# Performance work log

Hardware: AMD Instinct MI355X
Metric: run time of the kernel (lower is better)

Reference implementation:

```python
import jax, jax.numpy as jnp
import numpy as np
import math

D_MODEL = 2048
NUM_HEADS = 16
D_FF = 8192
HEAD_DIM = D_MODEL // NUM_HEADS
EPS = 1e-5


def _xavier(key, out_f, in_f):
    std = math.sqrt(2.0 / (in_f + out_f))
    return jax.random.normal(key, (out_f, in_f), dtype=jnp.float32) * std


def setup_inputs() -> dict:
    key = jax.random.key(0)
    ks = jax.random.split(key, 8)
    x = jax.random.normal(ks[0], (2, 2048, D_MODEL), dtype=jnp.float32)
    return {
        "x": x,
        "Wq": _xavier(ks[1], D_MODEL, D_MODEL),
        "Wk": _xavier(ks[2], D_MODEL, D_MODEL),
        "Wv": _xavier(ks[3], D_MODEL, D_MODEL),
        "Wo": _xavier(ks[4], D_MODEL, D_MODEL),
        "W1": _xavier(ks[5], D_FF, D_MODEL),
        "W2": _xavier(ks[6], D_MODEL, D_FF),
        "g1": jnp.ones((D_MODEL,), jnp.float32),
        "b1": jnp.zeros((D_MODEL,), jnp.float32),
        "g2": jnp.ones((D_MODEL,), jnp.float32),
        "b2": jnp.zeros((D_MODEL,), jnp.float32),
    }


def _ternary(w):
    # per-tensor abs-mean threshold -> {-1, 0, 1}
    abs_w = jnp.abs(w)
    thr = jnp.mean(abs_w)
    return jnp.where(abs_w > thr, jnp.sign(w), jnp.zeros_like(w))


def _tlin(x, w):
    # F.linear with ternarized weight [out, in], no bias
    return jnp.einsum("bsi,oi->bso", x, _ternary(w))


def _layernorm(x, g, b):
    mu = jnp.mean(x, axis=-1, keepdims=True)
    var = jnp.mean(jnp.square(x - mu), axis=-1, keepdims=True)
    return (x - mu) * jax.lax.rsqrt(var + EPS) * g + b


def reference(x, Wq, Wk, Wv, Wo, W1, W2, g1, b1, g2, b2):
    B, S, D = x.shape
    H, Hd = NUM_HEADS, HEAD_DIM
    q = _tlin(x, Wq).reshape(B, S, H, Hd).transpose(0, 2, 1, 3)  # bhsd
    k = _tlin(x, Wk).reshape(B, S, H, Hd).transpose(0, 2, 1, 3)
    v = _tlin(x, Wv).reshape(B, S, H, Hd).transpose(0, 2, 1, 3)
    scores = jnp.einsum("bhqd,bhkd->bhqk", q, k) / math.sqrt(Hd)
    probs = jax.nn.softmax(scores, axis=-1)
    attn = jnp.einsum("bhqk,bhkd->bhqd", probs, v)
    attn = attn.transpose(0, 2, 1, 3).reshape(B, S, D)
    attn = _tlin(attn, Wo)
    x = _layernorm(x + attn, g1, b1)  # dropout is identity in eval
    ff = _tlin(jax.nn.relu(_tlin(x, W1)), W2)
    x = _layernorm(x + ff, g2, b2)
    return x
```

## Files before the change

kernel.cpp:

```cpp
#include <hip/hip_runtime.h>
#include <hip/hip_bf16.h>

typedef __bf16 bf16_t;
typedef __bf16 bf16x8 __attribute__((ext_vector_type(8)));
typedef __bf16 bf16x4 __attribute__((ext_vector_type(4)));
typedef float f32x4 __attribute__((ext_vector_type(4)));
typedef int i32x4 __attribute__((ext_vector_type(4)));

__device__ __forceinline__ f32x4 mfma16(bf16x8 a, bf16x8 b, f32x4 c) {
  return __builtin_amdgcn_mfma_f32_16x16x32_bf16(a, b, c, 0, 0, 0);
}

__device__ __forceinline__ void gload16(const void* g, void* l) {
  __builtin_amdgcn_global_load_lds(
      (const __attribute__((address_space(1))) void*)g,
      (__attribute__((address_space(3))) void*)l, 16, 0, 0);
}

__global__ void abssum_all(const float* __restrict__ W0, const float* __restrict__ W1_,
                           const float* __restrict__ W2_, const float* __restrict__ W3,
                           const float* __restrict__ W4, const float* __restrict__ W5,
                           double* __restrict__ partial) {
  __shared__ double sd[256];
  const int w = blockIdx.y, tid = threadIdx.x;
  const float* W = (w == 0) ? W0 : (w == 1) ? W1_ : (w == 2) ? W2_ : (w == 3) ? W3 : (w == 4) ? W4 : W5;
  const int n4 = (w < 4) ? 1048576 : 4194304;
  double s = 0.0;
  for (int i = blockIdx.x * 256 + tid; i < n4; i += 262144) {
    float4 v = ((const float4*)W)[i];
    s += (double)fabsf(v.x); s += (double)fabsf(v.y);
    s += (double)fabsf(v.z); s += (double)fabsf(v.w);
  }
  sd[tid] = s; __syncthreads();
  for (int st = 128; st > 0; st >>= 1) { if (tid < st) sd[tid] += sd[tid + st]; __syncthreads(); }
  if (tid == 0) partial[w * 1024 + blockIdx.x] = sd[0];
}

__global__ void abssum_fin(const double* __restrict__ partial, double* __restrict__ sums) {
  __shared__ double sd[256];
  const int tid = threadIdx.x;
  const double* p = partial + blockIdx.x * 1024;
  double s = p[tid] + p[tid + 256] + p[tid + 512] + p[tid + 768];
  sd[tid] = s; __syncthreads();
  for (int st = 128; st > 0; st >>= 1) { if (tid < st) sd[tid] += sd[tid + st]; __syncthreads(); }
  if (tid == 0) sums[blockIdx.x] = sd[0];
}

__global__ void ternarize4(const float* __restrict__ W0, const float* __restrict__ W1_,
                           const float* __restrict__ W2_, const float* __restrict__ W3,
                           bf16_t* __restrict__ out, const double* __restrict__ sums) {
  const int w = blockIdx.x >> 12;
  const float* W = (w == 0) ? W0 : (w == 1) ? W1_ : (w == 2) ? W2_ : W3;
  const double thr = sums[w] / 4194304.0;
  const int i = (blockIdx.x & 4095) * 256 + threadIdx.x;
  float4 v = ((const float4*)W)[i];
  bf16x4 o;
  float t;
  t = ((double)fabsf(v.x) > thr) ? (v.x > 0.f ? 1.f : -1.f) : 0.f; o[0] = (bf16_t)t;
  t = ((double)fabsf(v.y) > thr) ? (v.y > 0.f ? 1.f : -1.f) : 0.f; o[1] = (bf16_t)t;
  t = ((double)fabsf(v.z) > thr) ? (v.z > 0.f ? 1.f : -1.f) : 0.f; o[2] = (bf16_t)t;
  t = ((double)fabsf(v.w) > thr) ? (v.w > 0.f ? 1.f : -1.f) : 0.f; o[3] = (bf16_t)t;
  *(bf16x4*)&out[(size_t)w * 4194304 + (size_t)i * 4] = o;
}

__global__ void ternarize_k(const float* __restrict__ W, bf16_t* __restrict__ out,
                            const double* __restrict__ sum, double n) {
  const double thr = sum[0] / n;
  const int i = blockIdx.x * 256 + threadIdx.x;
  float4 v = ((const float4*)W)[i];
  bf16x4 o;
  float t;
  t = ((double)fabsf(v.x) > thr) ? (v.x > 0.f ? 1.f : -1.f) : 0.f; o[0] = (bf16_t)t;
  t = ((double)fabsf(v.y) > thr) ? (v.y > 0.f ? 1.f : -1.f) : 0.f; o[1] = (bf16_t)t;
  t = ((double)fabsf(v.z) > thr) ? (v.z > 0.f ? 1.f : -1.f) : 0.f; o[2] = (bf16_t)t;
  t = ((double)fabsf(v.w) > thr) ? (v.w > 0.f ? 1.f : -1.f) : 0.f; o[3] = (bf16_t)t;
  *(bf16x4*)&out[(size_t)i * 4] = o;
}

__global__ void split_x_k(const float* __restrict__ X, bf16_t* __restrict__ xh, bf16_t* __restrict__ xl) {
  const int i = blockIdx.x * 256 + threadIdx.x;
  float4 v = ((const float4*)X)[i];
  bf16x4 h, l;
  h[0] = (bf16_t)v.x; l[0] = (bf16_t)(v.x - (float)h[0]);
  h[1] = (bf16_t)v.y; l[1] = (bf16_t)(v.y - (float)h[1]);
  h[2] = (bf16_t)v.z; l[2] = (bf16_t)(v.z - (float)h[2]);
  h[3] = (bf16_t)v.w; l[3] = (bf16_t)(v.w - (float)h[3]);
  *(bf16x4*)&xh[(size_t)i * 4] = h;
  *(bf16x4*)&xl[(size_t)i * 4] = l;
}

template <int EPI, bool SPLITA>
__global__ __launch_bounds__(512, 2) void gemmP(
    const bf16_t* __restrict__ Ah, const bf16_t* __restrict__ Al,
    const bf16_t* __restrict__ Bw,
    void* __restrict__ C0, void* __restrict__ C1,
    int M, int N, int K) {
  constexpr int BM = SPLITA ? 64 : 128;
  constexpr int MREP = SPLITA ? 2 : 4;
  constexpr int ABUF = BM * 64;
  constexpr int BBUF = 256 * 64;
  __shared__ __align__(16) bf16_t sA[3][ABUF];
  __shared__ __align__(16) bf16_t sA2[SPLITA ? 3 : 1][SPLITA ? ABUF : 8];
  __shared__ __align__(16) bf16_t sB[3][BBUF];

  const int tid = threadIdx.x;
  const int wid = tid >> 6, lane = tid & 63, lr = lane & 15, lg = lane >> 4;
  const int wr = wid >> 2, wc = wid & 3;
  const size_t Ks = (size_t)K;

  const int nwg = gridDim.x * gridDim.y;
  const int bid0 = blockIdx.y * gridDim.x + blockIdx.x;
  const int swz = (bid0 & 7) * (nwg >> 3) + (bid0 >> 3);
  const int bx = swz % gridDim.x, by = swz / gridDim.x;
  const size_t m0 = (size_t)by * BM, n0 = (size_t)bx * 256;
  const int nt = K / 64;

  f32x4 acc[MREP][4] = {};

  auto STAGEH = [&](int bi, int kt, int half) {
    const size_t ko = (size_t)kt * 64;
    if (half == 0) {
#pragma unroll
      for (int i = 0; i < BM / 64; i++) {
        const int t = i * 512 + tid;
        const int r = t >> 3;
        const int su = (t & 7) ^ (r & 7);
        const int lo = (i * 512 + wid * 64) * 8;
        gload16(Ah + (m0 + r) * Ks + ko + su * 8, (void*)&sA[bi][lo]);
        if constexpr (SPLITA) gload16(Al + (m0 + r) * Ks + ko + su * 8, (void*)&sA2[bi][lo]);
      }
      {
        const int r = tid >> 3;
        const int su = (tid & 7) ^ (r & 7);
        gload16(Bw + (n0 + r) * Ks + ko + su * 8, (void*)&sB[bi][(wid * 64) * 8]);
      }
    } else {
#pragma unroll
      for (int i = 1; i < 4; i++) {
        const int t = i * 512 + tid;
        const int r = t >> 3;
        const int su = (t & 7) ^ (r & 7);
        gload16(Bw + (n0 + r) * Ks + ko + su * 8, (void*)&sB[bi][(i * 512 + wid * 64) * 8]);
      }
    }
  };
  auto LDA = [&](const bf16_t* base, int m, int k) -> bf16x8 {
    const int row = wr * (BM / 2) + m * 16 + lr;
    const int u = (k * 4 + lg) ^ (lr & 7);
    return *(const bf16x8*)&base[row * 64 + u * 8];
  };
  auto LDB = [&](const bf16_t* base, int n, int k) -> bf16x8 {
    const int row = wc * 64 + n * 16 + lr;
    const int u = (k * 4 + lg) ^ (lr & 7);
    return *(const bf16x8*)&base[row * 64 + u * 8];
  };

  STAGEH(0, 0, 0); STAGEH(0, 0, 1);
  STAGEH(1, 1, 0); STAGEH(1, 1, 1);
  asm volatile("s_waitcnt vmcnt(6)" ::: "memory");
  __builtin_amdgcn_s_barrier();

  int bc = 0, bs = 2;
  for (int kt = 0; kt < nt; kt++) {
    const bool pf = (kt + 2 < nt);
    bf16x8 a[MREP][2], bfr[4][2];
#pragma unroll
    for (int m = 0; m < MREP; m++)
#pragma unroll
      for (int k = 0; k < 2; k++) a[m][k] = LDA(&sA[bc][0], m, k);
    if constexpr (SPLITA) {
#pragma unroll
      for (int n = 0; n < 4; n++)
#pragma unroll
        for (int k = 0; k < 2; k++) bfr[n][k] = LDB(&sB[bc][0], n, k);
    } else {
#pragma unroll
      for (int n = 0; n < 2; n++)
#pragma unroll
        for (int k = 0; k < 2; k++) bfr[n][k] = LDB(&sB[bc][0], n, k);
    }
    if (pf) STAGEH(bs, kt + 2, 0);
    __builtin_amdgcn_s_barrier();
    asm volatile("s_waitcnt lgkmcnt(0)" ::: "memory");
    __builtin_amdgcn_sched_barrier(0);
    __builtin_amdgcn_s_setprio(1);
    if constexpr (SPLITA) {
#pragma unroll
      for (int k = 0; k < 2; k++)
#pragma unroll
        for (int m = 0; m < MREP; m++)
#pragma unroll
          for (int n = 0; n < 4; n++) acc[m][n] = mfma16(a[m][k], bfr[n][k], acc[m][n]);
    } else {
#pragma unroll
      for (int k = 0; k < 2; k++)
#pragma unroll
        for (int m = 0; m < MREP; m++)
#pragma unroll
          for (int n = 0; n < 2; n++) acc[m][n] = mfma16(a[m][k], bfr[n][k], acc[m][n]);
    }
    __builtin_amdgcn_s_setprio(0);
    __builtin_amdgcn_s_barrier();
    if constexpr (SPLITA) {
#pragma unroll
      for (int m = 0; m < MREP; m++)
#pragma unroll
        for (int k = 0; k < 2; k++) a[m][k] = LDA(&sA2[bc][0], m, k);
    } else {
#pragma unroll
      for (int n = 0; n < 2; n++)
#pragma unroll
        for (int k = 0; k < 2; k++) bfr[n + 2][k] = LDB(&sB[bc][0], n + 2, k);
    }
    if (pf) STAGEH(bs, kt + 2, 1);
    if (kt + 1 < nt) {
      if (pf) asm volatile("s_waitcnt vmcnt(6)" ::: "memory");
      else    asm volatile("s_waitcnt vmcnt(0)" ::: "memory");
    }
    __builtin_amdgcn_s_barrier();
    asm volatile("s_waitcnt lgkmcnt(0)" ::: "memory");
    __builtin_amdgcn_sched_barrier(0);
    __builtin_amdgcn_s_setprio(1);
    if constexpr (SPLITA) {
#pragma unroll
      for (int k = 0; k < 2; k++)
#pragma unroll
        for (int m = 0; m < MREP; m++)
#pragma unroll
          for (int n = 0; n < 4; n++) acc[m][n] = mfma16(a[m][k], bfr[n][k], acc[m][n]);
    } else {
#pragma unroll
      for (int k = 0; k < 2; k++)
#pragma unroll
        for (int m = 0; m < MREP; m++)
#pragma unroll
          for (int n = 0; n < 2; n++) acc[m][n + 2] = mfma16(a[m][k], bfr[n + 2][k], acc[m][n + 2]);
    }
    __builtin_amdgcn_s_setprio(0);
    __builtin_amdgcn_s_barrier();
    bc = (bc + 1 == 3) ? 0 : bc + 1;
    bs = (bs + 1 == 3) ? 0 : bs + 1;
  }

  const int row0 = (int)m0 + wr * (BM / 2), colb = (int)n0 + wc * 64;
#pragma unroll
  for (int m = 0; m < MREP; m++)
#pragma unroll
    for (int n = 0; n < 4; n++)
#pragma unroll
      for (int j = 0; j < 4; j++) {
        const int r = row0 + m * 16 + lg * 4 + j;
        const int c = colb + n * 16 + lr;
        const float v = acc[m][n][j];
        if constexpr (EPI == 0) {
          bf16_t hi = (bf16_t)v;
          ((bf16_t*)C0)[(size_t)r * N + c] = hi;
          ((bf16_t*)C1)[(size_t)r * N + c] = (bf16_t)(v - (float)hi);
        } else if constexpr (EPI == 1) {
          const int bb = r >> 11, ss = r & 2047;
          ((bf16_t*)C0)[((size_t)bb * 2048 + c) * 2048 + ss] = (bf16_t)v;
        } else if constexpr (EPI == 2) {
          ((float*)C0)[(size_t)r * N + c] = v;
        } else {
          ((bf16_t*)C0)[(size_t)r * N + c] = (bf16_t)fmaxf(v, 0.f);
        }
      }
  (void)M;
}

template <int EPI>
__global__ __launch_bounds__(512, 2) void gemm256(
    const bf16_t* __restrict__ A, const bf16_t* __restrict__ Bw,
    void* __restrict__ C0, int M, int N, int K) {
  __shared__ __align__(16) bf16_t sA[2][256 * 64];
  __shared__ __align__(16) bf16_t sB[2][256 * 64];
  const int tid = threadIdx.x;
  const int wid = tid >> 6, lane = tid & 63, lr = lane & 15, lg = lane >> 4;
  const int wr = wid >> 2, wc = wid & 3;
  const size_t Ks = (size_t)K;
  const int nwg = gridDim.x * gridDim.y;
  const int bid0 = blockIdx.y * gridDim.x + blockIdx.x;
  const int swz = (bid0 & 7) * (nwg >> 3) + (bid0 >> 3);
  const int bx = swz % gridDim.x, by = swz / gridDim.x;
  const size_t m0 = (size_t)by * 256, n0 = (size_t)bx * 256;
  const int nt = K / 64;
  const bf16_t* Abase = A + m0 * Ks;
  const bf16_t* Bbase = Bw + n0 * Ks;

  f32x4 acc[8][4] = {};

  auto SG = [&](const bf16_t* base, bf16_t* dst, int kt, int h) {
    const size_t ko = (size_t)kt * 64;
#pragma unroll
    for (int i = 0; i < 2; i++) {
      const int e = (2 * h + i) * 512 + tid;
      const int r = e >> 3;
      const int su = (tid & 7) ^ (r & 7);
      gload16(base + (size_t)r * Ks + ko + su * 8,
              (void*)&dst[((2 * h + i) * 512 + wid * 64) * 8]);
    }
  };
  auto LDA = [&](int bi, int m, int k) -> bf16x8 {
    const int row = wr * 128 + m * 16 + lr;
    const int u = (k * 4 + lg) ^ (lr & 7);
    return *(const bf16x8*)&sA[bi][row * 64 + u * 8];
  };
  auto LDB = [&](int bi, int n, int k) -> bf16x8 {
    const int row = wc * 64 + n * 16 + lr;
    const int u = (k * 4 + lg) ^ (lr & 7);
    return *(const bf16x8*)&sB[bi][row * 64 + u * 8];
  };

  SG(Abase, sA[0], 0, 0); SG(Abase, sA[0], 0, 1);
  SG(Bbase, sB[0], 0, 0); SG(Bbase, sB[0], 0, 1);
  SG(Bbase, sB[1], 1, 0); SG(Bbase, sB[1], 1, 1); SG(Abase, sA[1], 1, 0);
  asm volatile("s_waitcnt vmcnt(6)" ::: "memory");
  __builtin_amdgcn_s_barrier();

  for (int kt = 0; kt < nt; kt++) {
    const int bi = kt & 1, bn = bi ^ 1;
    bf16x8 a[4][2], b[4][2];
#pragma unroll
    for (int m = 0; m < 4; m++)
#pragma unroll
      for (int k = 0; k < 2; k++) a[m][k] = LDA(bi, m, k);
#pragma unroll
    for (int n = 0; n < 2; n++)
#pragma unroll
      for (int k = 0; k < 2; k++) b[n][k] = LDB(bi, n, k);
    if (kt + 1 < nt) SG(Abase, sA[bn], kt + 1, 1);
    __builtin_amdgcn_s_barrier();
    asm volatile("s_waitcnt lgkmcnt(0)" ::: "memory");
    __builtin_amdgcn_sched_barrier(0);
    __builtin_amdgcn_s_setprio(1);
#pragma unroll
    for (int k = 0; k < 2; k++)
#pragma unroll
      for (int m = 0; m < 4; m++)
#pragma unroll
        for (int n = 0; n < 2; n++) acc[m][n] = mfma16(a[m][k], b[n][k], acc[m][n]);
    __builtin_amdgcn_s_setprio(0);
    __builtin_amdgcn_s_barrier();
#pragma unroll
    for (int n = 0; n < 2; n++)
#pragma unroll
      for (int k = 0; k < 2; k++) b[n + 2][k] = LDB(bi, n + 2, k);
    if (kt + 2 < nt) SG(Bbase, sB[bi], kt + 2, 0);
    __builtin_amdgcn_s_barrier();
    asm volatile("s_waitcnt lgkmcnt(0)" ::: "memory");
    __builtin_amdgcn_sched_barrier(0);
    __builtin_amdgcn_s_setprio(1);
#pragma unroll
    for (int k = 0; k < 2; k++)
#pragma unroll
      for (int m = 0; m < 4; m++)
#pragma unroll
        for (int n = 0; n < 2; n++) acc[m][n + 2] = mfma16(a[m][k], b[n + 2][k], acc[m][n + 2]);
    __builtin_amdgcn_s_setprio(0);
    __builtin_amdgcn_s_barrier();
#pragma unroll
    for (int m = 0; m < 4; m++)
#pragma unroll
      for (int k = 0; k < 2; k++) a[m][k] = LDA(bi, m + 4, k);
    if (kt + 2 < nt) SG(Bbase, sB[bi], kt + 2, 1);
    __builtin_amdgcn_s_barrier();
    asm volatile("s_waitcnt lgkmcnt(0)" ::: "memory");
    __builtin_amdgcn_sched_barrier(0);
    __builtin_amdgcn_s_setprio(1);
#pragma unroll
    for (int k = 0; k < 2; k++)
#pragma unroll
      for (int m = 0; m < 4; m++)
#pragma unroll
        for (int n = 0; n < 2; n++) acc[m + 4][n + 2] = mfma16(a[m][k], b[n + 2][k], acc[m + 4][n + 2]);
    __builtin_amdgcn_s_setprio(0);
    __builtin_amdgcn_s_barrier();
    if (kt + 2 < nt) SG(Abase, sA[bi], kt + 2, 0);
    __builtin_amdgcn_s_setprio(1);
#pragma unroll
    for (int k = 0; k < 2; k++)
#pragma unroll
      for (int m = 0; m < 4; m++)
#pragma unroll
        for (int n = 0; n < 2; n++) acc[m + 4][n] = mfma16(a[m][k], b[n][k], acc[m + 4][n]);
    __builtin_amdgcn_s_setprio(0);
    if (kt + 1 < nt) {
      if (kt + 2 < nt) asm volatile("s_waitcnt vmcnt(6)" ::: "memory");
      else             asm volatile("s_waitcnt vmcnt(0)" ::: "memory");
    }
    __builtin_amdgcn_s_barrier();
  }

  const int row0 = (int)m0 + wr * 128, colb = (int)n0 + wc * 64;
#pragma unroll
  for (int m = 0; m < 8; m++)
#pragma unroll
    for (int n = 0; n < 4; n++)
#pragma unroll
      for (int j = 0; j < 4; j++) {
        const int r = row0 + m * 16 + lg * 4 + j;
        const int c = colb + n * 16 + lr;
        const float v = acc[m][n][j];
        if constexpr (EPI == 2) {
          ((float*)C0)[(size_t)r * N + c] = v;
        } else {
          ((bf16_t*)C0)[(size_t)r * N + c] = (bf16_t)fmaxf(v, 0.f);
        }
      }
  (void)M;
}

__global__ __launch_bounds__(256, 2) void attn_k(
    const bf16_t* __restrict__ qh, const bf16_t* __restrict__ ql,
    const bf16_t* __restrict__ kh, const bf16_t* __restrict__ kl,
    const bf16_t* __restrict__ vT, bf16_t* __restrict__ out) {
  __shared__ __align__(16) bf16_t sKh[2 * 8192];
  __shared__ __align__(16) bf16_t sKl[2 * 8192];
  __shared__ __align__(16) bf16_t plds[4][2048];

  const int fid = blockIdx.y * 16 + blockIdx.x;
  const int qt = fid >> 5;
  const int bh = (fid & 7) * 4 + ((fid >> 3) & 3);
  const int b = bh >> 4, h = bh & 15;
  const int wv = threadIdx.x >> 6, lane = threadIdx.x & 63, lr = lane & 15, lg = lane >> 4;
  const size_t tok0 = (size_t)b * 2048 + qt * 128 + wv * 16;
  bf16_t* pw = &plds[wv][0];

  auto STAGE = [&](int bufi, int kv0n) {
#pragma unroll
    for (int i = 0; i < 4; i++) {
      const int tt = wv * 4 + i;
      const int r = tt * 4 + (lane >> 4);
      const int ce = ((lane & 15) ^ (r & 7)) * 8;
      const size_t gofs = ((size_t)b * 2048 + kv0n + r) * 4096 + h * 128 + ce;
      gload16(kh + gofs, (void*)&sKh[bufi * 8192 + tt * 512]);
      gload16(kl + gofs, (void*)&sKl[bufi * 8192 + tt * 512]);
    }
  };

  bf16x8 qhf[2][4], qlf[2][4];
#pragma unroll
  for (int t = 0; t < 2; t++) {
    const bf16_t* qp = qh + (tok0 + t * 64 + lr) * 4096 + h * 128 + lg * 8;
    const bf16_t* qp2 = ql + (tok0 + t * 64 + lr) * 4096 + h * 128 + lg * 8;
#pragma unroll
    for (int ks = 0; ks < 4; ks++) {
      qhf[t][ks] = *(const bf16x8*)(qp + ks * 32);
      qlf[t][ks] = *(const bf16x8*)(qp2 + ks * 32);
    }
  }
  f32x4 oacc[2][8] = {};
  float mrun[2] = {-1e30f, -1e30f};
  float lrun[2] = {0.f, 0.f};
  const bf16_t* vbase = vT + ((size_t)b * 2048 + h * 128) * 2048;
  const float sc = 0.08838834764831845f;
  const int swz8 = 2 * (lr & 7);

  STAGE(0, 0);
  for (int c = 0; c < 32; c++) {
    const int kv0 = c * 64;
    if (c + 1 < 32) {
      STAGE((c + 1) & 1, kv0 + 64);
      asm volatile("s_waitcnt vmcnt(8)" ::: "memory");
    } else {
      asm volatile("s_waitcnt vmcnt(0)" ::: "memory");
    }
    __builtin_amdgcn_s_barrier();

    const int bufo = (c & 1) * 8192;
    f32x4 s[2][4] = {};
    __builtin_amdgcn_s_setprio(1);
#pragma unroll
    for (int nb = 0; nb < 4; nb++) {
      const int rbase = bufo + (nb * 16 + lr) * 128;
#pragma unroll
      for (int ks = 0; ks < 4; ks++) {
        const int u = (((ks * 4 + lg) ^ (lr & 7)) * 8);
        bf16x8 kf = *(const bf16x8*)&sKh[rbase + u];
        bf16x8 kg = *(const bf16x8*)&sKl[rbase + u];
        s[0][nb] = mfma16(kf, qhf[0][ks], s[0][nb]);
        s[1][nb] = mfma16(kf, qhf[1][ks], s[1][nb]);
        s[0][nb] = mfma16(kf, qlf[0][ks], s[0][nb]);
        s[1][nb] = mfma16(kf, qlf[1][ks], s[1][nb]);
        s[0][nb] = mfma16(kg, qhf[0][ks], s[0][nb]);
        s[1][nb] = mfma16(kg, qhf[1][ks], s[1][nb]);
      }
    }
    __builtin_amdgcn_s_setprio(0);

    float resc[2];
    bool skip[2];
#pragma unroll
    for (int t = 0; t < 2; t++) {
#pragma unroll
      for (int nb = 0; nb < 4; nb++) s[t][nb] *= sc;
      f32x4 m4 = __builtin_elementwise_max(
          __builtin_elementwise_max(s[t][0], s[t][1]),
          __builtin_elementwise_max(s[t][2], s[t][3]));
      float mx = fmaxf(fmaxf(m4[0], m4[1]), fmaxf(m4[2], m4[3]));
      mx = fmaxf(mx, __shfl_xor(mx, 16));
      mx = fmaxf(mx, __shfl_xor(mx, 32));
      skip[t] = (__all(mx <= mrun[t] + 8.f) != 0);
      float rs_ = 1.f;
      if (!skip[t]) {
        const float mnew = fmaxf(mrun[t], mx);
        rs_ = __expf(mrun[t] - mnew);
        mrun[t] = mnew;
      }
      resc[t] = rs_;
      float ls = 0.f;
#pragma unroll
      for (int nb = 0; nb < 4; nb++) {
        bf16x4 pk;
#pragma unroll
        for (int j = 0; j < 4; j++) {
          const float p = __expf(s[t][nb][j] - mrun[t]);
          ls += p;
          pk[j] = (bf16_t)p;
        }
        const int s8 = (4 * nb + lg) ^ swz8;
        *(bf16x4*)&pw[t * 1024 + lr * 64 + s8 * 4] = pk;
      }
      ls += __shfl_xor(ls, 16);
      ls += __shfl_xor(ls, 32);
      lrun[t] = lrun[t] * rs_ + ls;
    }
    asm volatile("s_waitcnt lgkmcnt(0)" ::: "memory");
    __builtin_amdgcn_sched_barrier(0);
    bf16x8 pfr[2][2];
#pragma unroll
    for (int t = 0; t < 2; t++)
#pragma unroll
      for (int kc = 0; kc < 2; kc++) {
        const int se = (8 * kc + 2 * lg) ^ swz8;
        pfr[t][kc] = *(const bf16x8*)&pw[t * 1024 + lr * 64 + se * 4];
      }
    if (!skip[0]) {
#pragma unroll
      for (int dt = 0; dt < 8; dt++) oacc[0][dt] *= resc[0];
    }
    if (!skip[1]) {
#pragma unroll
      for (int dt = 0; dt < 8; dt++) oacc[1][dt] *= resc[1];
    }

    const bf16_t* vp = vbase + kv0 + lg * 8;
    __builtin_amdgcn_s_setprio(1);
#pragma unroll
    for (int dt = 0; dt < 8; dt++) {
      const bf16_t* vr = vp + (size_t)(dt * 16 + lr) * 2048;
      bf16x8 v0 = *(const bf16x8*)(vr);
      bf16x8 v1 = *(const bf16x8*)(vr + 32);
      oacc[0][dt] = mfma16(v0, pfr[0][0], oacc[0][dt]);
      oacc[1][dt] = mfma16(v0, pfr[1][0], oacc[1][dt]);
      oacc[0][dt] = mfma16(v1, pfr[0][1], oacc[0][dt]);
      oacc[1][dt] = mfma16(v1, pfr[1][1], oacc[1][dt]);
    }
    __builtin_amdgcn_s_setprio(0);
    asm volatile("" ::: "memory");
    __builtin_amdgcn_s_barrier();
  }

  {
    bf16_t* ep = &sKh[wv * 2176];
    const int q = lane >> 2, c4 = lane & 3;
    const int qs = 2 * (q & 7);
#pragma unroll
    for (int t = 0; t < 2; t++) {
      const float inv = 1.f / lrun[t];
#pragma unroll
      for (int dt = 0; dt < 8; dt++) {
        bf16x4 pk;
#pragma unroll
        for (int j = 0; j < 4; j++) pk[j] = (bf16_t)(oacc[t][dt][j] * inv);
        const int s5 = (4 * dt + lg) ^ swz8;
        *(bf16x4*)&ep[lr * 136 + s5 * 4] = pk;
      }
      asm volatile("s_waitcnt lgkmcnt(0)" ::: "memory");
      __builtin_amdgcn_sched_barrier(0);
      bf16_t* orow = out + (tok0 + t * 64 + q) * 2048 + h * 128 + c4 * 32;
#pragma unroll
      for (int i = 0; i < 4; i++) {
        const int se = (c4 * 8 + 2 * i) ^ qs;
        bf16x8 vv = *(const bf16x8*)&ep[q * 136 + se * 4];
        *(bf16x8*)(orow + i * 8) = vv;
      }
      asm volatile("s_waitcnt lgkmcnt(0)" ::: "memory");
    }
  }
}

__global__ __launch_bounds__(256) void ln_k(
    const float* __restrict__ X, const float* __restrict__ R,
    const float* __restrict__ G, const float* __restrict__ Bt,
    float* __restrict__ O32, bf16_t* __restrict__ O16) {
  const int t = blockIdx.x, tid = threadIdx.x;
  const float4* xp = (const float4*)(X + (size_t)t * 2048);
  const float4* rp = (const float4*)(R + (size_t)t * 2048);
  float4 v0 = xp[tid], w0 = rp[tid];
  float4 v1 = xp[tid + 256], w1 = rp[tid + 256];
  v0.x += w0.x; v0.y += w0.y; v0.z += w0.z; v0.w += w0.w;
  v1.x += w1.x; v1.y += w1.y; v1.z += w1.z; v1.w += w1.w;
  float sum = v0.x + v0.y + v0.z + v0.w + v1.x + v1.y + v1.z + v1.w;
  float sq = v0.x * v0.x + v0.y * v0.y + v0.z * v0.z + v0.w * v0.w +
             v1.x * v1.x + v1.y * v1.y + v1.z * v1.z + v1.w * v1.w;
  for (int d = 1; d < 64; d <<= 1) { sum += __shfl_xor(sum, d); sq += __shfl_xor(sq, d); }
  __shared__ float s1[4], s2[4];
  const int wv = tid >> 6, lane = tid & 63;
  if (lane == 0) { s1[wv] = sum; s2[wv] = sq; }
  __syncthreads();
  const float tot = s1[0] + s1[1] + s1[2] + s1[3];
  const float tsq = s2[0] + s2[1] + s2[2] + s2[3];
  const float mu = tot * (1.f / 2048.f);
  const float var = tsq * (1.f / 2048.f) - mu * mu;
  const float rs = 1.f / sqrtf(var + 1e-5f);
  const float4* gp = (const float4*)G;
  const float4* bp = (const float4*)Bt;
  float4 g0 = gp[tid], g1v = gp[tid + 256], b0 = bp[tid], b1v = bp[tid + 256];
  float4 o0, o1;
  o0.x = (v0.x - mu) * rs * g0.x + b0.x; o0.y = (v0.y - mu) * rs * g0.y + b0.y;
  o0.z = (v0.z - mu) * rs * g0.z + b0.z; o0.w = (v0.w - mu) * rs * g0.w + b0.w;
  o1.x = (v1.x - mu) * rs * g1v.x + b1v.x; o1.y = (v1.y - mu) * rs * g1v.y + b1v.y;
  o1.z = (v1.z - mu) * rs * g1v.z + b1v.z; o1.w = (v1.w - mu) * rs * g1v.w + b1v.w;
  ((float4*)(O32 + (size_t)t * 2048))[tid] = o0;
  ((float4*)(O32 + (size_t)t * 2048))[tid + 256] = o1;
  if (O16) {
    bf16x4 h0, h1;
    h0[0] = (bf16_t)o0.x; h0[1] = (bf16_t)o0.y; h0[2] = (bf16_t)o0.z; h0[3] = (bf16_t)o0.w;
    h1[0] = (bf16_t)o1.x; h1[1] = (bf16_t)o1.y; h1[2] = (bf16_t)o1.z; h1[3] = (bf16_t)o1.w;
    *(bf16x4*)&O16[(size_t)t * 2048 + tid * 4] = h0;
    *(bf16x4*)&O16[(size_t)t * 2048 + 1024 + tid * 4] = h1;
  }
}

extern "C" void kernel_launch(void* const* d_in, const int* in_sizes, int n_in,
                              void* d_out, int out_size, void* d_ws, size_t ws_size,
                              hipStream_t stream) {
  const float* x  = (const float*)d_in[0];
  const float* Wq = (const float*)d_in[1];
  const float* Wk = (const float*)d_in[2];
  const float* Wv = (const float*)d_in[3];
  const float* Wo = (const float*)d_in[4];
  const float* W1 = (const float*)d_in[5];
  const float* W2 = (const float*)d_in[6];
  const float* g1 = (const float*)d_in[7];
  const float* b1 = (const float*)d_in[8];
  const float* g2 = (const float*)d_in[9];
  const float* b2 = (const float*)d_in[10];
  float* out = (float*)d_out;
  char* ws = (char*)d_ws;

  constexpr size_t SZB = (size_t)4096 * 2048 * 2;
  bf16_t* xh  = (bf16_t*)(ws + 0 * SZB);
  bf16_t* xl  = (bf16_t*)(ws + 1 * SZB);
  bf16_t* qkh = (bf16_t*)(ws + 2 * SZB);
  bf16_t* qkl = (bf16_t*)(ws + 4 * SZB);
  bf16_t* vt  = (bf16_t*)(ws + 6 * SZB);
  bf16_t* at  = (bf16_t*)(ws + 7 * SZB);
  float* o32  = (float*)(ws + 8 * SZB);
  bf16_t* wt  = (bf16_t*)(ws + 8 * SZB + (size_t)4096 * 2048 * 4);
  double* red = (double*)(ws + 8 * SZB + (size_t)4096 * 2048 * 4 + (size_t)8192 * 2048 * 2);
  double* sums = red + 8192;
  float* h1 = (float*)ws;
  bf16_t* h1b = qkh;
  bf16_t* f1 = (bf16_t*)(ws + 4 * SZB);
  float* g32 = o32;
  (void)in_sizes; (void)n_in; (void)out_size; (void)ws_size;

  abssum_all<<<dim3(1024, 6), 256, 0, stream>>>(Wq, Wk, Wv, Wo, W1, W2, red);
  abssum_fin<<<6, 256, 0, stream>>>(red, sums);
  split_x_k<<<8192, 256, 0, stream>>>(x, xh, xl);
  ternarize4<<<16384, 256, 0, stream>>>(Wq, Wk, Wv, Wo, wt, sums);

  gemmP<0, true><<<dim3(16, 64), 512, 0, stream>>>(xh, xl, wt, qkh, qkl, 4096, 4096, 2048);
  gemmP<1, false><<<dim3(8, 32), 512, 0, stream>>>(xh, nullptr, wt + 8388608, vt, nullptr, 4096, 2048, 2048);
  attn_k<<<dim3(16, 32), 256, 0, stream>>>(qkh, qkl, qkh + 2048, qkl + 2048, vt, at);
  gemmP<2, false><<<dim3(8, 32), 512, 0, stream>>>(at, nullptr, wt + 12582912, o32, nullptr, 4096, 2048, 2048);
  ln_k<<<4096, 256, 0, stream>>>(x, o32, g1, b1, h1, h1b);
  ternarize_k<<<16384, 256, 0, stream>>>(W1, wt, sums + 4, 16777216.0);
  gemm256<3><<<dim3(32, 16), 512, 0, stream>>>(h1b, wt, f1, 4096, 8192, 2048);
  ternarize_k<<<16384, 256, 0, stream>>>(W2, wt, sums + 5, 16777216.0);
  gemmP<2, false><<<dim3(8, 32), 512, 0, stream>>>(f1, nullptr, wt, g32, nullptr, 4096, 2048, 8192);
  ln_k<<<4096, 256, 0, stream>>>(h1, g32, g2, b2, out, nullptr);
}
```

Baseline: 812.1 us.

## Fold hi/lo split of x into doubled-K GEMM using 256x256 tile kernel

```diff
diff --git a/kernel.cpp b/kernel.cpp
--- a/kernel.cpp
+++ b/kernel.cpp
@@ -77,31 +77,26 @@
   *(bf16x4*)&out[(size_t)i * 4] = o;
 }
 
-__global__ void split_x_k(const float* __restrict__ X, bf16_t* __restrict__ xh, bf16_t* __restrict__ xl) {
+__global__ void split_x_k(const float* __restrict__ X, bf16_t* __restrict__ xhl) {
   const int i = blockIdx.x * 256 + threadIdx.x;
+  const int t = i >> 9, col = (i & 511) * 4;
   float4 v = ((const float4*)X)[i];
   bf16x4 h, l;
   h[0] = (bf16_t)v.x; l[0] = (bf16_t)(v.x - (float)h[0]);
   h[1] = (bf16_t)v.y; l[1] = (bf16_t)(v.y - (float)h[1]);
   h[2] = (bf16_t)v.z; l[2] = (bf16_t)(v.z - (float)h[2]);
   h[3] = (bf16_t)v.w; l[3] = (bf16_t)(v.w - (float)h[3]);
-  *(bf16x4*)&xh[(size_t)i * 4] = h;
-  *(bf16x4*)&xl[(size_t)i * 4] = l;
-}
-
-template <int EPI, bool SPLITA>
+  *(bf16x4*)&xhl[(size_t)t * 4096 + col] = h;
+  *(bf16x4*)&xhl[(size_t)t * 4096 + 2048 + col] = l;
+}
+
+template <int EPI>
 __global__ __launch_bounds__(512, 2) void gemmP(
-    const bf16_t* __restrict__ Ah, const bf16_t* __restrict__ Al,
-    const bf16_t* __restrict__ Bw,
-    void* __restrict__ C0, void* __restrict__ C1,
-    int M, int N, int K) {
-  constexpr int BM = SPLITA ? 64 : 128;
-  constexpr int MREP = SPLITA ? 2 : 4;
-  constexpr int ABUF = BM * 64;
-  constexpr int BBUF = 256 * 64;
-  __shared__ __align__(16) bf16_t sA[3][ABUF];
-  __shared__ __align__(16) bf16_t sA2[SPLITA ? 3 : 1][SPLITA ? ABUF : 8];
-  __shared__ __align__(16) bf16_t sB[3][BBUF];
+    const bf16_t* __restrict__ Ah, const bf16_t* __restrict__ Bw,
+    void* __restrict__ C0, int N, int K, int lda) {
+  constexpr int BM = 128;
+  __shared__ __align__(16) bf16_t sA[3][BM * 64];
+  __shared__ __align__(16) bf16_t sB[3][256 * 64];
 
   const int tid = threadIdx.x;
   const int wid = tid >> 6, lane = tid & 63, lr = lane & 15, lg = lane >> 4;
@@ -115,19 +110,18 @@
   const size_t m0 = (size_t)by * BM, n0 = (size_t)bx * 256;
   const int nt = K / 64;
 
-  f32x4 acc[MREP][4] = {};
+  f32x4 acc[4][4] = {};
 
   auto STAGEH = [&](int bi, int kt, int half) {
     const size_t ko = (size_t)kt * 64;
     if (half == 0) {
 #pragma unroll
-      for (int i = 0; i < BM / 64; i++) {
+      for (int i = 0; i < 2; i++) {
         const int t = i * 512 + tid;
         const int r = t >> 3;
         const int su = (t & 7) ^ (r & 7);
         const int lo = (i * 512 + wid * 64) * 8;
-        gload16(Ah + (m0 + r) * Ks + ko + su * 8, (void*)&sA[bi][lo]);
-        if constexpr (SPLITA) gload16(Al + (m0 + r) * Ks + ko + su * 8, (void*)&sA2[bi][lo]);
+        gload16(Ah + (m0 + r) * (size_t)lda + ko + su * 8, (void*)&sA[bi][lo]);
       }
       {
         const int r = tid >> 3;
@@ -145,7 +139,7 @@
     }
   };
   auto LDA = [&](const bf16_t* base, int m, int k) -> bf16x8 {
-    const int row = wr * (BM / 2) + m * 16 + lr;
+    const int row = wr * 64 + m * 16 + lr;
     const int u = (k * 4 + lg) ^ (lr & 7);
     return *(const bf16x8*)&base[row * 64 + u * 8];
   };
@@ -163,55 +157,32 @@
   int bc = 0, bs = 2;
   for (int kt = 0; kt < nt; kt++) {
     const bool pf = (kt + 2 < nt);
-    bf16x8 a[MREP][2], bfr[4][2];
-#pragma unroll
-    for (int m = 0; m < MREP; m++)
+    bf16x8 a[4][2], bfr[4][2];
+#pragma unroll
+    for (int m = 0; m < 4; m++)
 #pragma unroll
       for (int k = 0; k < 2; k++) a[m][k] = LDA(&sA[bc][0], m, k);
-    if constexpr (SPLITA) {
-#pragma unroll
-      for (int n = 0; n < 4; n++)
-#pragma unroll
-        for (int k = 0; k < 2; k++) bfr[n][k] = LDB(&sB[bc][0], n, k);
-    } else {
-#pragma unroll
-      for (int n = 0; n < 2; n++)
-#pragma unroll
-        for (int k = 0; k < 2; k++) bfr[n][k] = LDB(&sB[bc][0], n, k);
-    }
+#pragma unroll
+    for (int n = 0; n < 2; n++)
+#pragma unroll
+      for (int k = 0; k < 2; k++) bfr[n][k] = LDB(&sB[bc][0], n, k);
     if (pf) STAGEH(bs, kt + 2, 0);
     __builtin_amdgcn_s_barrier();
     asm volatile("s_waitcnt lgkmcnt(0)" ::: "memory");
     __builtin_amdgcn_sched_barrier(0);
     __builtin_amdgcn_s_setprio(1);
-    if constexpr (SPLITA) {
-#pragma unroll
-      for (int k = 0; k < 2; k++)
-#pragma unroll
-        for (int m = 0; m < MREP; m++)
-#pragma unroll
-          for (int n = 0; n < 4; n++) acc[m][n] = mfma16(a[m][k], bfr[n][k], acc[m][n]);
-    } else {
-#pragma unroll
-      for (int k = 0; k < 2; k++)
-#pragma unroll
-        for (int m = 0; m < MREP; m++)
-#pragma unroll
-          for (int n = 0; n < 2; n++) acc[m][n] = mfma16(a[m][k], bfr[n][k], acc[m][n]);
-    }
-    __builtin_amdgcn_s_setprio(0);
-    __builtin_amdgcn_s_barrier();
-    if constexpr (SPLITA) {
-#pragma unroll
-      for (int m = 0; m < MREP; m++)
-#pragma unroll
-        for (int k = 0; k < 2; k++) a[m][k] = LDA(&sA2[bc][0], m, k);
-    } else {
-#pragma unroll
-      for (int n = 0; n < 2; n++)
-#pragma unroll
-        for (int k = 0; k < 2; k++) bfr[n + 2][k] = LDB(&sB[bc][0], n + 2, k);
-    }
+#pragma unroll
+    for (int k = 0; k < 2; k++)
+#pragma unroll
+      for (int m = 0; m < 4; m++)
+#pragma unroll
+        for (int n = 0; n < 2; n++) acc[m][n] = mfma16(a[m][k], bfr[n][k], acc[m][n]);
+    __builtin_amdgcn_s_setprio(0);
+    __builtin_amdgcn_s_barrier();
+#pragma unroll
+    for (int n = 0; n < 2; n++)
+#pragma unroll
+      for (int k = 0; k < 2; k++) bfr[n + 2][k] = LDB(&sB[bc][0], n + 2, k);
     if (pf) STAGEH(bs, kt + 2, 1);
     if (kt + 1 < nt) {
       if (pf) asm volatile("s_waitcnt vmcnt(6)" ::: "memory");
@@ -221,30 +192,21 @@
     asm volatile("s_waitcnt lgkmcnt(0)" ::: "memory");
     __builtin_amdgcn_sched_barrier(0);
     __builtin_amdgcn_s_setprio(1);
-    if constexpr (SPLITA) {
-#pragma unroll
-      for (int k = 0; k < 2; k++)
-#pragma unroll
-        for (int m = 0; m < MREP; m++)
-#pragma unroll
-          for (int n = 0; n < 4; n++) acc[m][n] = mfma16(a[m][k], bfr[n][k], acc[m][n]);
-    } else {
-#pragma unroll
-      for (int k = 0; k < 2; k++)
-#pragma unroll
-        for (int m = 0; m < MREP; m++)
-#pragma unroll
-          for (int n = 0; n < 2; n++) acc[m][n + 2] = mfma16(a[m][k], bfr[n + 2][k], acc[m][n + 2]);
-    }
+#pragma unroll
+    for (int k = 0; k < 2; k++)
+#pragma unroll
+      for (int m = 0; m < 4; m++)
+#pragma unroll
+        for (int n = 0; n < 2; n++) acc[m][n + 2] = mfma16(a[m][k], bfr[n + 2][k], acc[m][n + 2]);
     __builtin_amdgcn_s_setprio(0);
     __builtin_amdgcn_s_barrier();
     bc = (bc + 1 == 3) ? 0 : bc + 1;
     bs = (bs + 1 == 3) ? 0 : bs + 1;
   }
 
-  const int row0 = (int)m0 + wr * (BM / 2), colb = (int)n0 + wc * 64;
-#pragma unroll
-  for (int m = 0; m < MREP; m++)
+  const int row0 = (int)m0 + wr * 64, colb = (int)n0 + wc * 64;
+#pragma unroll
+  for (int m = 0; m < 4; m++)
 #pragma unroll
     for (int n = 0; n < 4; n++)
 #pragma unroll
@@ -252,11 +214,7 @@
         const int r = row0 + m * 16 + lg * 4 + j;
         const int c = colb + n * 16 + lr;
         const float v = acc[m][n][j];
-        if constexpr (EPI == 0) {
-          bf16_t hi = (bf16_t)v;
-          ((bf16_t*)C0)[(size_t)r * N + c] = hi;
-          ((bf16_t*)C1)[(size_t)r * N + c] = (bf16_t)(v - (float)hi);
-        } else if constexpr (EPI == 1) {
+        if constexpr (EPI == 1) {
           const int bb = r >> 11, ss = r & 2047;
           ((bf16_t*)C0)[((size_t)bb * 2048 + c) * 2048 + ss] = (bf16_t)v;
         } else if constexpr (EPI == 2) {
@@ -265,38 +223,37 @@
           ((bf16_t*)C0)[(size_t)r * N + c] = (bf16_t)fmaxf(v, 0.f);
         }
       }
-  (void)M;
 }
 
 template <int EPI>
 __global__ __launch_bounds__(512, 2) void gemm256(
     const bf16_t* __restrict__ A, const bf16_t* __restrict__ Bw,
-    void* __restrict__ C0, int M, int N, int K) {
+    void* __restrict__ C0, void* __restrict__ C1,
+    int N, int K, int lda, int ldb) {
   __shared__ __align__(16) bf16_t sA[2][256 * 64];
   __shared__ __align__(16) bf16_t sB[2][256 * 64];
   const int tid = threadIdx.x;
   const int wid = tid >> 6, lane = tid & 63, lr = lane & 15, lg = lane >> 4;
   const int wr = wid >> 2, wc = wid & 3;
-  const size_t Ks = (size_t)K;
   const int nwg = gridDim.x * gridDim.y;
   const int bid0 = blockIdx.y * gridDim.x + blockIdx.x;
   const int swz = (bid0 & 7) * (nwg >> 3) + (bid0 >> 3);
   const int bx = swz % gridDim.x, by = swz / gridDim.x;
   const size_t m0 = (size_t)by * 256, n0 = (size_t)bx * 256;
   const int nt = K / 64;
-  const bf16_t* Abase = A + m0 * Ks;
-  const bf16_t* Bbase = Bw + n0 * Ks;
+  const bf16_t* Abase = A + m0 * (size_t)lda;
+  const bf16_t* Bbase = Bw + n0 * (size_t)ldb;
 
   f32x4 acc[8][4] = {};
 
-  auto SG = [&](const bf16_t* base, bf16_t* dst, int kt, int h) {
-    const size_t ko = (size_t)kt * 64;
+  auto SG = [&](const bf16_t* base, bf16_t* dst, int kt, int h, int ld) {
+    const size_t co = (size_t)((kt * 64) & (ld - 1));
 #pragma unroll
     for (int i = 0; i < 2; i++) {
       const int e = (2 * h + i) * 512 + tid;
       const int r = e >> 3;
       const int su = (tid & 7) ^ (r & 7);
-      gload16(base + (size_t)r * Ks + ko + su * 8,
+      gload16(base + (size_t)r * ld + co + su * 8,
               (void*)&dst[((2 * h + i) * 512 + wid * 64) * 8]);
     }
   };
@@ -311,9 +268,9 @@
     return *(const bf16x8*)&sB[bi][row * 64 + u * 8];
   };
 
-  SG(Abase, sA[0], 0, 0); SG(Abase, sA[0], 0, 1);
-  SG(Bbase, sB[0], 0, 0); SG(Bbase, sB[0], 0, 1);
-  SG(Bbase, sB[1], 1, 0); SG(Bbase, sB[1], 1, 1); SG(Abase, sA[1], 1, 0);
+  SG(Abase, sA[0], 0, 0, lda); SG(Abase, sA[0], 0, 1, lda);
+  SG(Bbase, sB[0], 0, 0, ldb); SG(Bbase, sB[0], 0, 1, ldb);
+  SG(Bbase, sB[1], 1, 0, ldb); SG(Bbase, sB[1], 1, 1, ldb); SG(Abase, sA[1], 1, 0, lda);
   asm volatile("s_waitcnt vmcnt(6)" ::: "memory");
   __builtin_amdgcn_s_barrier();
 
@@ -328,7 +285,7 @@
     for (int n = 0; n < 2; n++)
 #pragma unroll
       for (int k = 0; k < 2; k++) b[n][k] = LDB(bi, n, k);
-    if (kt + 1 < nt) SG(Abase, sA[bn], kt + 1, 1);
+    if (kt + 1 < nt) SG(Abase, sA[bn], kt + 1, 1, lda);
     __builtin_amdgcn_s_barrier();
     asm volatile("s_waitcnt lgkmcnt(0)" ::: "memory");
     __builtin_amdgcn_sched_barrier(0);
@@ -345,7 +302,7 @@
     for (int n = 0; n < 2; n++)
 #pragma unroll
       for (int k = 0; k < 2; k++) b[n + 2][k] = LDB(bi, n + 2, k);
-    if (kt + 2 < nt) SG(Bbase, sB[bi], kt + 2, 0);
+    if (kt + 2 < nt) SG(Bbase, sB[bi], kt + 2, 0, ldb);
     __builtin_amdgcn_s_barrier();
     asm volatile("s_waitcnt lgkmcnt(0)" ::: "memory");
     __builtin_amdgcn_sched_barrier(0);
@@ -362,7 +319,7 @@
     for (int m = 0; m < 4; m++)
 #pragma unroll
       for (int k = 0; k < 2; k++) a[m][k] = LDA(bi, m + 4, k);
-    if (kt + 2 < nt) SG(Bbase, sB[bi], kt + 2, 1);
+    if (kt + 2 < nt) SG(Bbase, sB[bi], kt + 2, 1, ldb);
     __builtin_amdgcn_s_barrier();
     asm volatile("s_waitcnt lgkmcnt(0)" ::: "memory");
     __builtin_amdgcn_sched_barrier(0);
@@ -375,7 +332,7 @@
         for (int n = 0; n < 2; n++) acc[m + 4][n + 2] = mfma16(a[m][k], b[n + 2][k], acc[m + 4][n + 2]);
     __builtin_amdgcn_s_setprio(0);
     __builtin_amdgcn_s_barrier();
-    if (kt + 2 < nt) SG(Abase, sA[bi], kt + 2, 0);
+    if (kt + 2 < nt) SG(Abase, sA[bi], kt + 2, 0, lda);
     __builtin_amdgcn_s_setprio(1);
 #pragma unroll
     for (int k = 0; k < 2; k++)
@@ -401,13 +358,14 @@
         const int r = row0 + m * 16 + lg * 4 + j;
         const int c = colb + n * 16 + lr;
         const float v = acc[m][n][j];
-        if constexpr (EPI == 2) {
-          ((float*)C0)[(size_t)r * N + c] = v;
+        if constexpr (EPI == 0) {
+          bf16_t hi = (bf16_t)v;
+          ((bf16_t*)C0)[(size_t)r * N + c] = hi;
+          ((bf16_t*)C1)[(size_t)r * N + c] = (bf16_t)(v - (float)hi);
         } else {
           ((bf16_t*)C0)[(size_t)r * N + c] = (bf16_t)fmaxf(v, 0.f);
         }
       }
-  (void)M;
 }
 
 __global__ __launch_bounds__(256, 2) void attn_k(
@@ -651,8 +609,7 @@
   char* ws = (char*)d_ws;
 
   constexpr size_t SZB = (size_t)4096 * 2048 * 2;
-  bf16_t* xh  = (bf16_t*)(ws + 0 * SZB);
-  bf16_t* xl  = (bf16_t*)(ws + 1 * SZB);
+  bf16_t* xhl = (bf16_t*)(ws + 0 * SZB);
   bf16_t* qkh = (bf16_t*)(ws + 2 * SZB);
   bf16_t* qkl = (bf16_t*)(ws + 4 * SZB);
   bf16_t* vt  = (bf16_t*)(ws + 6 * SZB);
@@ -669,17 +626,17 @@
 
   abssum_all<<<dim3(1024, 6), 256, 0, stream>>>(Wq, Wk, Wv, Wo, W1, W2, red);
   abssum_fin<<<6, 256, 0, stream>>>(red, sums);
-  split_x_k<<<8192, 256, 0, stream>>>(x, xh, xl);
+  split_x_k<<<8192, 256, 0, stream>>>(x, xhl);
   ternarize4<<<16384, 256, 0, stream>>>(Wq, Wk, Wv, Wo, wt, sums);
 
-  gemmP<0, true><<<dim3(16, 64), 512, 0, stream>>>(xh, xl, wt, qkh, qkl, 4096, 4096, 2048);
-  gemmP<1, false><<<dim3(8, 32), 512, 0, stream>>>(xh, nullptr, wt + 8388608, vt, nullptr, 4096, 2048, 2048);
+  gemm256<0><<<dim3(16, 16), 512, 0, stream>>>(xhl, wt, qkh, qkl, 4096, 4096, 4096, 2048);
+  gemmP<1><<<dim3(8, 32), 512, 0, stream>>>(xhl, wt + 8388608, vt, 2048, 2048, 4096);
   attn_k<<<dim3(16, 32), 256, 0, stream>>>(qkh, qkl, qkh + 2048, qkl + 2048, vt, at);
-  gemmP<2, false><<<dim3(8, 32), 512, 0, stream>>>(at, nullptr, wt + 12582912, o32, nullptr, 4096, 2048, 2048);
+  gemmP<2><<<dim3(8, 32), 512, 0, stream>>>(at, wt + 12582912, o32, 2048, 2048, 2048);
   ln_k<<<4096, 256, 0, stream>>>(x, o32, g1, b1, h1, h1b);
   ternarize_k<<<16384, 256, 0, stream>>>(W1, wt, sums + 4, 16777216.0);
-  gemm256<3><<<dim3(32, 16), 512, 0, stream>>>(h1b, wt, f1, 4096, 8192, 2048);
+  gemm256<3><<<dim3(32, 16), 512, 0, stream>>>(h1b, wt, f1, nullptr, 8192, 2048, 2048, 2048);
   ternarize_k<<<16384, 256, 0, stream>>>(W2, wt, sums + 5, 16777216.0);
-  gemmP<2, false><<<dim3(8, 32), 512, 0, stream>>>(f1, nullptr, wt, g32, nullptr, 4096, 2048, 8192);
+  gemmP<2><<<dim3(8, 32), 512, 0, stream>>>(f1, wt, g32, 2048, 8192, 8192);
   ln_k<<<4096, 256, 0, stream>>>(h1, g32, g2, b2, out, nullptr);
 }
```

Measured after the change: 795.2 us. 2.1% less time.
